# Kernel tuning notes

Hardware: AMD Instinct MI355X
Metric: run time of the kernel (lower is better)

The kernel has to match this reference:

```python
import jax, jax.numpy as jnp
import numpy as np

N, IN_DIM, SLOT_DIM, HID = 524288, 64, 64, 128
NUM_SLOTS, NUM_ITERS = 3, 2
EPS = 1e-8


def _ln(x, g, b):
    m = jnp.mean(x, -1, keepdims=True)
    v = jnp.mean((x - m) ** 2, -1, keepdims=True)
    return (x - m) * jax.lax.rsqrt(v + 1e-5) * g + b


def _gru(x, h, wih, whh, bih, bhh):
    # torch.nn.GRUCell: gates ordered (r, z, n)
    gi = x @ wih.T + bih
    gh = h @ whh.T + bhh
    ir, iz, inn = jnp.split(gi, 3, -1)
    hr, hz, hn = jnp.split(gh, 3, -1)
    r = jax.nn.sigmoid(ir + hr)
    z = jax.nn.sigmoid(iz + hz)
    n = jnp.tanh(inn + r * hn)
    return (1.0 - z) * n + z * h


def setup_inputs() -> dict:
    key = jax.random.key(0)
    ks = jax.random.split(key, 40)
    f32 = jnp.float32
    d = {}
    d['x'] = jax.random.normal(ks[0], (N, IN_DIM), f32)
    d['noise_fg'] = jax.random.normal(ks[1], (NUM_SLOTS - 1, SLOT_DIM), f32)
    d['noise_bg'] = jax.random.normal(ks[2], (1, SLOT_DIM), f32)
    d['ln_in_g'] = jnp.ones((IN_DIM,), f32); d['ln_in_b'] = jnp.zeros((IN_DIM,), f32)
    d['mu_fg'] = jax.random.normal(ks[3], (1, SLOT_DIM), f32)
    d['logsig_fg'] = jax.random.normal(ks[4], (1, SLOT_DIM), f32) * 0.1
    d['mu_bg'] = jax.random.normal(ks[5], (1, SLOT_DIM), f32)
    d['logsig_bg'] = jax.random.normal(ks[6], (1, SLOT_DIM), f32) * 0.1
    d['Wk'] = jax.random.normal(ks[7], (SLOT_DIM, IN_DIM), f32) * 0.1
    d['Wv'] = jax.random.normal(ks[8], (SLOT_DIM, IN_DIM), f32) * 0.1
    d['lnq_fg_g'] = jnp.ones((SLOT_DIM,), f32); d['lnq_fg_b'] = jnp.zeros((SLOT_DIM,), f32)
    d['Wq_fg'] = jax.random.normal(ks[9], (SLOT_DIM, SLOT_DIM), f32) * 0.1
    d['lnq_bg_g'] = jnp.ones((SLOT_DIM,), f32); d['lnq_bg_b'] = jnp.zeros((SLOT_DIM,), f32)
    d['Wq_bg'] = jax.random.normal(ks[10], (SLOT_DIM, SLOT_DIM), f32) * 0.1
    d['gfg_wih'] = jax.random.normal(ks[11], (3 * SLOT_DIM, SLOT_DIM), f32) * 0.1
    d['gfg_whh'] = jax.random.normal(ks[12], (3 * SLOT_DIM, SLOT_DIM), f32) * 0.1
    d['gfg_bih'] = jnp.zeros((3 * SLOT_DIM,), f32); d['gfg_bhh'] = jnp.zeros((3 * SLOT_DIM,), f32)
    d['gbg_wih'] = jax.random.normal(ks[13], (3 * SLOT_DIM, SLOT_DIM), f32) * 0.1
    d['gbg_whh'] = jax.random.normal(ks[14], (3 * SLOT_DIM, SLOT_DIM), f32) * 0.1
    d['gbg_bih'] = jnp.zeros((3 * SLOT_DIM,), f32); d['gbg_bhh'] = jnp.zeros((3 * SLOT_DIM,), f32)
    d['mfg_ln_g'] = jnp.ones((SLOT_DIM,), f32); d['mfg_ln_b'] = jnp.zeros((SLOT_DIM,), f32)
    d['mfg_w1'] = jax.random.normal(ks[15], (HID, SLOT_DIM), f32) * 0.1
    d['mfg_b1'] = jnp.zeros((HID,), f32)
    d['mfg_w2'] = jax.random.normal(ks[16], (SLOT_DIM, HID), f32) * 0.1
    d['mfg_b2'] = jnp.zeros((SLOT_DIM,), f32)
    d['mbg_ln_g'] = jnp.ones((SLOT_DIM,), f32); d['mbg_ln_b'] = jnp.zeros((SLOT_DIM,), f32)
    d['mbg_w1'] = jax.random.normal(ks[17], (HID, SLOT_DIM), f32) * 0.1
    d['mbg_b1'] = jnp.zeros((HID,), f32)
    d['mbg_w2'] = jax.random.normal(ks[18], (SLOT_DIM, HID), f32) * 0.1
    d['mbg_b2'] = jnp.zeros((SLOT_DIM,), f32)
    return d


def _forward(x, noise_fg, noise_bg, ln_in_g, ln_in_b, mu_fg, logsig_fg, mu_bg, logsig_bg,
             Wk, Wv, lnq_fg_g, lnq_fg_b, Wq_fg, lnq_bg_g, lnq_bg_b, Wq_bg,
             gfg_wih, gfg_whh, gfg_bih, gfg_bhh, gbg_wih, gbg_whh, gbg_bih, gbg_bhh,
             mfg_ln_g, mfg_ln_b, mfg_w1, mfg_b1, mfg_w2, mfg_b2,
             mbg_ln_g, mbg_ln_b, mbg_w1, mbg_b1, mbg_w2, mbg_b2):
    scale = SLOT_DIM ** -0.5
    slot_fg = mu_fg + jnp.exp(logsig_fg) * noise_fg        # [K-1, D]
    slot_bg = mu_bg + jnp.exp(logsig_bg) * noise_bg        # [1, D]
    xn = _ln(x, ln_in_g, ln_in_b)
    k = xn @ Wk.T                                          # [N, D]
    v = xn @ Wv.T                                          # [N, D]
    attn = None
    for _ in range(NUM_ITERS):
        q_fg = (_ln(slot_fg, lnq_fg_g, lnq_fg_b) @ Wq_fg.T) * scale
        q_bg = (_ln(slot_bg, lnq_bg_g, lnq_bg_b) @ Wq_bg.T) * scale
        logits = jnp.concatenate([k @ q_bg.T, k @ q_fg.T], axis=-1)  # [N, K]
        attn = jax.nn.softmax(logits, axis=-1)
        attn_bg, attn_fg = attn[:, 0:1], attn[:, 1:]
        w_bg = attn_bg + EPS
        w_bg = w_bg / jnp.sum(w_bg, axis=-2, keepdims=True)
        upd_bg = w_bg.T @ v                                # [1, D]
        w_fg = attn_fg + EPS
        w_fg = w_fg / jnp.sum(w_fg, axis=-2, keepdims=True)
        upd_fg = w_fg.T @ v                                # [K-1, D]
        slot_bg = _gru(upd_bg, slot_bg, gbg_wih, gbg_whh, gbg_bih, gbg_bhh)
        slot_fg = _gru(upd_fg, slot_fg, gfg_wih, gfg_whh, gfg_bih, gfg_bhh)
        slot_bg = slot_bg + (jax.nn.relu(_ln(slot_bg, mbg_ln_g, mbg_ln_b) @ mbg_w1.T + mbg_b1) @ mbg_w2.T + mbg_b2)
        slot_fg = slot_fg + (jax.nn.relu(_ln(slot_fg, mfg_ln_g, mfg_ln_b) @ mfg_w1.T + mfg_b1) @ mfg_w2.T + mfg_b2)
    slots = jnp.concatenate([slot_bg, slot_fg], axis=0)    # [K, D]
    return slots, attn.T                                   # [K,D], [K,N]


def reference(x, noise_fg, noise_bg, ln_in_g, ln_in_b, mu_fg, logsig_fg, mu_bg, logsig_bg,
              Wk, Wv, lnq_fg_g, lnq_fg_b, Wq_fg, lnq_bg_g, lnq_bg_b, Wq_bg,
              gfg_wih, gfg_whh, gfg_bih, gfg_bhh, gbg_wih, gbg_whh, gbg_bih, gbg_bhh,
              mfg_ln_g, mfg_ln_b, mfg_w1, mfg_b1, mfg_w2, mfg_b2,
              mbg_ln_g, mbg_ln_b, mbg_w1, mbg_b1, mbg_w2, mbg_b2):
    return _forward(x, noise_fg, noise_bg, ln_in_g, ln_in_b, mu_fg, logsig_fg, mu_bg, logsig_bg,
                    Wk, Wv, lnq_fg_g, lnq_fg_b, Wq_fg, lnq_bg_g, lnq_bg_b, Wq_bg,
                    gfg_wih, gfg_whh, gfg_bih, gfg_bhh, gbg_wih, gbg_whh, gbg_bih, gbg_bhh,
                    mfg_ln_g, mfg_ln_b, mfg_w1, mfg_b1, mfg_w2, mfg_b2,
                    mbg_ln_g, mbg_ln_b, mbg_w1, mbg_b1, mbg_w2, mbg_b2)
```

## Files before the change

kernel.cpp:

```cpp
#include <hip/hip_runtime.h>
#include <math.h>

#define NROWS 524288
constexpr float EPSW = 1e-8f;

constexpr int OFF_WVT     = 0;
constexpr int OFF_WIHT_BG = 4096;
constexpr int OFF_WHHT_BG = 16384;
constexpr int OFF_WIHT_FG = 28672;
constexpr int OFF_WHHT_FG = 40960;
constexpr int OFF_W1T_BG  = 53248;
constexpr int OFF_W2T_BG  = 61440;
constexpr int OFF_W1T_FG  = 69632;
constexpr int OFF_W2T_FG  = 77824;
constexpr int OFF_WQT_BG  = 86016;
constexpr int OFF_WQT_FG  = 90112;
constexpr int OFF_SLOTS   = 94208;
constexpr int OFF_QG      = 94400;
constexpr int OFF_QS      = 94784;
constexpr int OFF_M       = 94800;
constexpr int OFF_W       = 95184;
constexpr int OFF_CM      = 95190;

__device__ __forceinline__ float wave_sum(float v) {
#pragma unroll
  for (int m = 1; m < 64; m <<= 1) v += __shfl_xor(v, m, 64);
  return v;
}

struct TJob { const float* src; int RC; int Cshift; int dstOff; };
struct TArgs { TJob j[11]; };

__global__ void transpose_k(TArgs a, float* __restrict__ ws) {
  TJob jb = a.j[blockIdx.x];
  const int C = 1 << jb.Cshift;
  const int R = jb.RC >> jb.Cshift;
  float* dst = ws + jb.dstOff;
  for (int e = threadIdx.x; e < jb.RC; e += blockDim.x) {
    int r = e >> jb.Cshift;
    int c = e & (C - 1);
    dst[c * R + r] = jb.src[e];
  }
}

__device__ void emit_q(int lane, float snew,
                       const float* __restrict__ lnq_g, const float* __restrict__ lnq_b,
                       const float* __restrict__ WqT, const float* __restrict__ Wk,
                       const float* __restrict__ g_in, const float* __restrict__ b_in,
                       float* scratch ,
                       float* __restrict__ qg_out , float* __restrict__ qs_out , int s)
{
  float mean = wave_sum(snew) * (1.0f / 64.0f);
  float d = snew - mean;
  float var = wave_sum(d * d) * (1.0f / 64.0f);
  float lns = d * rsqrtf(var + 1e-5f) * lnq_g[lane] + lnq_b[lane];
  scratch[lane] = lns;
  float q = 0.f;
#pragma unroll
  for (int dd = 0; dd < 64; ++dd) q = fmaf(scratch[dd], WqT[dd * 64 + lane], q);
  q *= 0.125f;
  scratch[lane] = q;
  float qk = 0.f;
#pragma unroll
  for (int j = 0; j < 64; ++j) qk = fmaf(scratch[j], Wk[j * 64 + lane], qk);
  float qgv = qk * g_in[lane];
  qg_out[lane] = qgv;
  float QG = wave_sum(qgv);
  float QB = wave_sum(qk * b_in[lane]);
  if (lane == 0) { qs_out[s] = QG; qs_out[3 + s] = QB; }
}

__global__ void init_k(const float* __restrict__ noise_fg, const float* __restrict__ noise_bg,
                       const float* __restrict__ g_in, const float* __restrict__ b_in,
                       const float* __restrict__ mu_fg, const float* __restrict__ logsig_fg,
                       const float* __restrict__ mu_bg, const float* __restrict__ logsig_bg,
                       const float* __restrict__ lnq_fg_g, const float* __restrict__ lnq_fg_b,
                       const float* __restrict__ lnq_bg_g, const float* __restrict__ lnq_bg_b,
                       const float* __restrict__ Wk, float* __restrict__ ws)
{
  __shared__ float scratch[64];
  const int lane = threadIdx.x;
#pragma unroll
  for (int i = 0; i < 6; ++i) ws[OFF_M + i * 64 + lane] = 0.f;
  if (lane < 12) ws[OFF_W + lane] = 0.f;

  float s0 = mu_bg[lane] + __expf(logsig_bg[lane]) * noise_bg[lane];
  float s1 = mu_fg[lane] + __expf(logsig_fg[lane]) * noise_fg[lane];
  float s2 = mu_fg[lane] + __expf(logsig_fg[lane]) * noise_fg[64 + lane];
  ws[OFF_SLOTS + lane] = s0;
  ws[OFF_SLOTS + 64 + lane] = s1;
  ws[OFF_SLOTS + 128 + lane] = s2;

  emit_q(lane, s0, lnq_bg_g, lnq_bg_b, ws + OFF_WQT_BG, Wk, g_in, b_in, scratch,
         ws + OFF_QG + 0, ws + OFF_QS, 0);
  emit_q(lane, s1, lnq_fg_g, lnq_fg_b, ws + OFF_WQT_FG, Wk, g_in, b_in, scratch,
         ws + OFF_QG + 64, ws + OFF_QS, 1);
  emit_q(lane, s2, lnq_fg_g, lnq_fg_b, ws + OFF_WQT_FG, Wk, g_in, b_in, scratch,
         ws + OFF_QG + 128, ws + OFF_QS, 2);
}

template <int WRITE_OUT>
__launch_bounds__(192) __global__ void attn_pass_k(
    const float* __restrict__ x,
    const float* __restrict__ qg,
    const float* __restrict__ qs,
    float* __restrict__ M_out,
    float* __restrict__ W_out,
    float* __restrict__ CM_out,
    float* __restrict__ attn_out)
{
  __shared__ float  lx[3][64 * 65];
  __shared__ float4 lc[3][64];
  __shared__ float4 lqg4[48];
  __shared__ float  lsc[3][8];
  const int tid = threadIdx.x;
  const int wid = tid >> 6, lane = tid & 63;
  if (tid < 48) lqg4[tid] = ((const float4*)qg)[tid];
  __syncthreads();
  const float QG0 = qs[0], QG1 = qs[1], QG2 = qs[2];
  const float QB0 = qs[3], QB1 = qs[4], QB2 = qs[5];

  float accM0 = 0, accM1 = 0, accM2 = 0;
  float accW0 = 0, accW1 = 0, accW2 = 0;
  float accC0 = 0, accC1 = 0, accC2 = 0;
  float* lxw = lx[wid];
  const int nw = gridDim.x * 3;

  for (int chunk = blockIdx.x * 3 + wid; chunk < (NROWS / 64); chunk += nw) {
    const int n0 = chunk << 6;
    const float4* xp = (const float4*)(x + (size_t)n0 * 64);
#pragma unroll
    for (int i = 0; i < 16; ++i) {
      float4 v = xp[i * 64 + lane];
      int f = (i * 64 + lane) << 2;
      float* p = &lxw[(f >> 6) * 65 + (f & 63)];
      p[0] = v.x; p[1] = v.y; p[2] = v.z; p[3] = v.w;
    }
    const float* rowp = &lxw[lane * 65];
    float sum = 0.f, ssq = 0.f, da0 = 0.f, da1 = 0.f, da2 = 0.f;
#pragma unroll
    for (int i = 0; i < 16; ++i) {
      float x0 = rowp[4 * i], x1 = rowp[4 * i + 1], x2 = rowp[4 * i + 2], x3 = rowp[4 * i + 3];
      float4 q0 = lqg4[i], q1 = lqg4[16 + i], q2 = lqg4[32 + i];
      sum += (x0 + x1) + (x2 + x3);
      ssq = fmaf(x0, x0, fmaf(x1, x1, fmaf(x2, x2, fmaf(x3, x3, ssq))));
      da0 = fmaf(x0, q0.x, fmaf(x1, q0.y, fmaf(x2, q0.z, fmaf(x3, q0.w, da0))));
      da1 = fmaf(x0, q1.x, fmaf(x1, q1.y, fmaf(x2, q1.z, fmaf(x3, q1.w, da1))));
      da2 = fmaf(x0, q2.x, fmaf(x1, q2.y, fmaf(x2, q2.z, fmaf(x3, q2.w, da2))));
    }
    float mean = sum * 0.015625f;
    float var  = fmaf(ssq, 0.015625f, -mean * mean);
    float rs   = rsqrtf(var + 1e-5f);
    float l0 = fmaf(rs, da0 - mean * QG0, QB0);
    float l1 = fmaf(rs, da1 - mean * QG1, QB1);
    float l2 = fmaf(rs, da2 - mean * QG2, QB2);
    float mx = fmaxf(l0, fmaxf(l1, l2));
    float e0 = __expf(l0 - mx), e1 = __expf(l1 - mx), e2 = __expf(l2 - mx);
    float inv = 1.0f / (e0 + e1 + e2);
    float a0 = e0 * inv, a1 = e1 * inv, a2 = e2 * inv;
    if (WRITE_OUT) {
      attn_out[0 * NROWS + n0 + lane] = a0;
      attn_out[1 * NROWS + n0 + lane] = a1;
      attn_out[2 * NROWS + n0 + lane] = a2;
    }
    float aw0 = a0 + EPSW, aw1 = a1 + EPSW, aw2 = a2 + EPSW;
    accW0 += aw0; accW1 += aw1; accW2 += aw2;
    float c0 = aw0 * rs, c1 = aw1 * rs, c2 = aw2 * rs;
    accC0 = fmaf(c0, mean, accC0);
    accC1 = fmaf(c1, mean, accC1);
    accC2 = fmaf(c2, mean, accC2);
    lc[wid][lane] = make_float4(c0, c1, c2, 0.f);
#pragma unroll
    for (int r = 0; r < 64; ++r) {
      float4 c = lc[wid][r];
      float xv = lxw[r * 65 + lane];
      accM0 = fmaf(c.x, xv, accM0);
      accM1 = fmaf(c.y, xv, accM1);
      accM2 = fmaf(c.z, xv, accM2);
    }
  }

  accW0 = wave_sum(accW0); accW1 = wave_sum(accW1); accW2 = wave_sum(accW2);
  accC0 = wave_sum(accC0); accC1 = wave_sum(accC1); accC2 = wave_sum(accC2);
  if (lane == 0) {
    lsc[wid][0] = accW0; lsc[wid][1] = accW1; lsc[wid][2] = accW2;
    lsc[wid][3] = accC0; lsc[wid][4] = accC1; lsc[wid][5] = accC2;
  }
  __syncthreads();
  float* red = (float*)lc;
  red[wid * 192 + lane]        = accM0;
  red[wid * 192 + 64 + lane]   = accM1;
  red[wid * 192 + 128 + lane]  = accM2;
  __syncthreads();
  if (tid < 192) atomicAdd(&M_out[tid], red[tid] + red[192 + tid] + red[384 + tid]);
  if (tid < 6) {
    float v = lsc[0][tid] + lsc[1][tid] + lsc[2][tid];
    if (tid < 3) atomicAdd(&W_out[tid], v);
    else         atomicAdd(&CM_out[tid - 3], v);
  }
}

__launch_bounds__(192) __global__ void update_k(
    const float* __restrict__ g_in, const float* __restrict__ b_in,
    const float* __restrict__ gbg_bih, const float* __restrict__ gbg_bhh,
    const float* __restrict__ gfg_bih, const float* __restrict__ gfg_bhh,
    const float* __restrict__ mbg_ln_g, const float* __restrict__ mbg_ln_b,
    const float* __restrict__ mfg_ln_g, const float* __restrict__ mfg_ln_b,
    const float* __restrict__ mbg_b1, const float* __restrict__ mbg_b2,
    const float* __restrict__ mfg_b1, const float* __restrict__ mfg_b2,
    const float* __restrict__ lnq_fg_g, const float* __restrict__ lnq_fg_b,
    const float* __restrict__ lnq_bg_g, const float* __restrict__ lnq_bg_b,
    const float* __restrict__ Wk,
    float* __restrict__ ws, int set_in, int last, float* __restrict__ out_slots)
{
  __shared__ float sA[3][64], sU[3][64], sH[3][64], sHid[3][128];
  const int tid = threadIdx.x, wid = tid >> 6, lane = tid & 63;
  const bool bg = (wid == 0);
  const float* wihT = ws + (bg ? OFF_WIHT_BG : OFF_WIHT_FG);
  const float* whhT = ws + (bg ? OFF_WHHT_BG : OFF_WHHT_FG);
  const float* w1T  = ws + (bg ? OFF_W1T_BG : OFF_W1T_FG);
  const float* w2T  = ws + (bg ? OFF_W2T_BG : OFF_W2T_FG);
  const float* WqT  = ws + (bg ? OFF_WQT_BG : OFF_WQT_FG);
  const float* bih = bg ? gbg_bih : gfg_bih;
  const float* bhh = bg ? gbg_bhh : gfg_bhh;
  const float* mlg = bg ? mbg_ln_g : mfg_ln_g;
  const float* mlb = bg ? mbg_ln_b : mfg_ln_b;
  const float* b1  = bg ? mbg_b1 : mfg_b1;
  const float* b2  = bg ? mbg_b2 : mfg_b2;
  const float* lqg = bg ? lnq_bg_g : lnq_fg_g;
  const float* lqb = bg ? lnq_bg_b : lnq_fg_b;

  const float Wsum = ws[OFF_W + set_in * 3 + wid];
  const float CM   = ws[OFF_CM + set_in * 3 + wid];
  const float Mv   = ws[OFF_M + set_in * 192 + wid * 64 + lane];
  float m = g_in[lane] * (Mv - CM) + b_in[lane] * Wsum;
  sA[wid][lane] = m;
  __syncthreads();

  const float* WvT = ws + OFF_WVT;
  float upd = 0.f;
#pragma unroll
  for (int d = 0; d < 64; ++d) upd = fmaf(sA[wid][d], WvT[d * 64 + lane], upd);
  upd /= Wsum;

  float h = ws[OFF_SLOTS + wid * 64 + lane];
  sU[wid][lane] = upd; sH[wid][lane] = h;
  __syncthreads();

  float gi0 = bih[lane], gi1 = bih[64 + lane], gi2 = bih[128 + lane];
  float gh0 = bhh[lane], gh1 = bhh[64 + lane], gh2 = bhh[128 + lane];
#pragma unroll
  for (int d = 0; d < 64; ++d) {
    float u = sU[wid][d], hh = sH[wid][d];
    const float* wi = &wihT[d * 192];
    const float* wh = &whhT[d * 192];
    gi0 = fmaf(u, wi[lane], gi0);
    gi1 = fmaf(u, wi[64 + lane], gi1);
    gi2 = fmaf(u, wi[128 + lane], gi2);
    gh0 = fmaf(hh, wh[lane], gh0);
    gh1 = fmaf(hh, wh[64 + lane], gh1);
    gh2 = fmaf(hh, wh[128 + lane], gh2);
  }
  float r  = 1.f / (1.f + __expf(-(gi0 + gh0)));
  float z  = 1.f / (1.f + __expf(-(gi1 + gh1)));
  float nn = tanhf(fmaf(r, gh2, gi2));
  float hp = (1.f - z) * nn + z * h;

  float mean = wave_sum(hp) * (1.f / 64.f);
  float dv = hp - mean;
  float var = wave_sum(dv * dv) * (1.f / 64.f);
  float lnh = dv * rsqrtf(var + 1e-5f) * mlg[lane] + mlb[lane];
  __syncthreads();
  sA[wid][lane] = lnh;
  __syncthreads();
  float h1a = b1[lane], h1b = b1[64 + lane];
#pragma unroll
  for (int d = 0; d < 64; ++d) {
    float t = sA[wid][d];
    h1a = fmaf(t, w1T[d * 128 + lane], h1a);
    h1b = fmaf(t, w1T[d * 128 + 64 + lane], h1b);
  }
  h1a = fmaxf(h1a, 0.f); h1b = fmaxf(h1b, 0.f);
  sHid[wid][lane] = h1a; sHid[wid][64 + lane] = h1b;
  __syncthreads();
  float o = b2[lane];
#pragma unroll
  for (int j = 0; j < 128; ++j) o = fmaf(sHid[wid][j], w2T[j * 64 + lane], o);
  float snew = hp + o;
  ws[OFF_SLOTS + wid * 64 + lane] = snew;

  if (last) {
    out_slots[wid * 64 + lane] = snew;
  } else {
    int so = set_in ^ 1;
    emit_q(lane, snew, lqg, lqb, WqT, Wk, g_in, b_in, sA[wid],
           ws + OFF_QG + so * 192 + wid * 64, ws + OFF_QS + so * 6, wid);
  }
}

extern "C" void kernel_launch(void* const* d_in, const int* in_sizes, int n_in,
                              void* d_out, int out_size, void* d_ws, size_t ws_size,
                              hipStream_t stream)
{
  (void)in_sizes; (void)n_in; (void)out_size; (void)ws_size;
  const float* x         = (const float*)d_in[0];
  const float* noise_fg  = (const float*)d_in[1];
  const float* noise_bg  = (const float*)d_in[2];
  const float* ln_in_g   = (const float*)d_in[3];
  const float* ln_in_b   = (const float*)d_in[4];
  const float* mu_fg     = (const float*)d_in[5];
  const float* logsig_fg = (const float*)d_in[6];
  const float* mu_bg     = (const float*)d_in[7];
  const float* logsig_bg = (const float*)d_in[8];
  const float* Wk        = (const float*)d_in[9];
  const float* Wv        = (const float*)d_in[10];
  const float* lnq_fg_g  = (const float*)d_in[11];
  const float* lnq_fg_b  = (const float*)d_in[12];
  const float* Wq_fg     = (const float*)d_in[13];
  const float* lnq_bg_g  = (const float*)d_in[14];
  const float* lnq_bg_b  = (const float*)d_in[15];
  const float* Wq_bg     = (const float*)d_in[16];
  const float* gfg_wih   = (const float*)d_in[17];
  const float* gfg_whh   = (const float*)d_in[18];
  const float* gfg_bih   = (const float*)d_in[19];
  const float* gfg_bhh   = (const float*)d_in[20];
  const float* gbg_wih   = (const float*)d_in[21];
  const float* gbg_whh   = (const float*)d_in[22];
  const float* gbg_bih   = (const float*)d_in[23];
  const float* gbg_bhh   = (const float*)d_in[24];
  const float* mfg_ln_g  = (const float*)d_in[25];
  const float* mfg_ln_b  = (const float*)d_in[26];
  const float* mfg_w1    = (const float*)d_in[27];
  const float* mfg_b1    = (const float*)d_in[28];
  const float* mfg_w2    = (const float*)d_in[29];
  const float* mfg_b2    = (const float*)d_in[30];
  const float* mbg_ln_g  = (const float*)d_in[31];
  const float* mbg_ln_b  = (const float*)d_in[32];
  const float* mbg_w1    = (const float*)d_in[33];
  const float* mbg_b1    = (const float*)d_in[34];
  const float* mbg_w2    = (const float*)d_in[35];
  const float* mbg_b2    = (const float*)d_in[36];

  float* ws  = (float*)d_ws;
  float* out = (float*)d_out;

  TArgs ta;
  ta.j[0]  = {Wv,      64 * 64,  6, OFF_WVT};
  ta.j[1]  = {gbg_wih, 192 * 64, 6, OFF_WIHT_BG};
  ta.j[2]  = {gbg_whh, 192 * 64, 6, OFF_WHHT_BG};
  ta.j[3]  = {gfg_wih, 192 * 64, 6, OFF_WIHT_FG};
  ta.j[4]  = {gfg_whh, 192 * 64, 6, OFF_WHHT_FG};
  ta.j[5]  = {mbg_w1,  128 * 64, 6, OFF_W1T_BG};
  ta.j[6]  = {mbg_w2,  64 * 128, 7, OFF_W2T_BG};
  ta.j[7]  = {mfg_w1,  128 * 64, 6, OFF_W1T_FG};
  ta.j[8]  = {mfg_w2,  64 * 128, 7, OFF_W2T_FG};
  ta.j[9]  = {Wq_bg,   64 * 64,  6, OFF_WQT_BG};
  ta.j[10] = {Wq_fg,   64 * 64,  6, OFF_WQT_FG};
  transpose_k<<<11, 256, 0, stream>>>(ta, ws);

  init_k<<<1, 64, 0, stream>>>(noise_fg, noise_bg, ln_in_g, ln_in_b,
                               mu_fg, logsig_fg, mu_bg, logsig_bg,
                               lnq_fg_g, lnq_fg_b, lnq_bg_g, lnq_bg_b, Wk, ws);

  attn_pass_k<0><<<768, 192, 0, stream>>>(x, ws + OFF_QG, ws + OFF_QS,
                                          ws + OFF_M, ws + OFF_W, ws + OFF_CM, nullptr);
  update_k<<<1, 192, 0, stream>>>(ln_in_g, ln_in_b, gbg_bih, gbg_bhh, gfg_bih, gfg_bhh,
                                  mbg_ln_g, mbg_ln_b, mfg_ln_g, mfg_ln_b,
                                  mbg_b1, mbg_b2, mfg_b1, mfg_b2,
                                  lnq_fg_g, lnq_fg_b, lnq_bg_g, lnq_bg_b, Wk,
                                  ws, 0, 0, nullptr);
  attn_pass_k<1><<<768, 192, 0, stream>>>(x, ws + OFF_QG + 192, ws + OFF_QS + 6,
                                          ws + OFF_M + 192, ws + OFF_W + 3, ws + OFF_CM + 3,
                                          out + 192);
  update_k<<<1, 192, 0, stream>>>(ln_in_g, ln_in_b, gbg_bih, gbg_bhh, gfg_bih, gfg_bhh,
                                  mbg_ln_g, mbg_ln_b, mfg_ln_g, mfg_ln_b,
                                  mbg_b1, mbg_b2, mfg_b1, mfg_b2,
                                  lnq_fg_g, lnq_fg_b, lnq_bg_g, lnq_bg_b, Wk,
                                  ws, 1, 1, out);
}
```

Measured before the change: 527.6 us.

## Restructure attention pass into register-resident streaming and fuse slot update via last-block

The attention pass drops its LDS transpose of x. Each row is now split across 16 lanes holding float4 values, reduced with xor-shuffles, and the next chunk is prefetched into registers, using 1024 blocks of 256 threads. The per-iteration slot update (GRU, MLP, next query) now runs inside the attention kernel: a done-counter atomic picks the last block to do it. The transpose and init kernels are merged into one prep kernel, which also transposes Wq in shared memory. This cuts kernel launches and LDS traffic, at the cost of more shuffles, higher register pressure, and a serialized tail in the final block.

```diff
diff --git a/kernel.cpp b/kernel.cpp
--- a/kernel.cpp
+++ b/kernel.cpp
@@ -21,6 +21,7 @@
 constexpr int OFF_M       = 94800;
 constexpr int OFF_W       = 95184;
 constexpr int OFF_CM      = 95190;
+constexpr int OFF_DONE    = 95200;
 
 __device__ __forceinline__ float wave_sum(float v) {
 #pragma unroll
@@ -28,27 +29,12 @@
   return v;
 }
 
-struct TJob { const float* src; int RC; int Cshift; int dstOff; };
-struct TArgs { TJob j[11]; };
-
-__global__ void transpose_k(TArgs a, float* __restrict__ ws) {
-  TJob jb = a.j[blockIdx.x];
-  const int C = 1 << jb.Cshift;
-  const int R = jb.RC >> jb.Cshift;
-  float* dst = ws + jb.dstOff;
-  for (int e = threadIdx.x; e < jb.RC; e += blockDim.x) {
-    int r = e >> jb.Cshift;
-    int c = e & (C - 1);
-    dst[c * R + r] = jb.src[e];
-  }
-}
-
 __device__ void emit_q(int lane, float snew,
                        const float* __restrict__ lnq_g, const float* __restrict__ lnq_b,
-                       const float* __restrict__ WqT, const float* __restrict__ Wk,
+                       const float* WqT, int qstride, const float* __restrict__ Wk,
                        const float* __restrict__ g_in, const float* __restrict__ b_in,
-                       float* scratch ,
-                       float* __restrict__ qg_out , float* __restrict__ qs_out , int s)
+                       float* scratch,
+                       float* __restrict__ qg_out, float* __restrict__ qs_out, int s)
 {
   float mean = wave_sum(snew) * (1.0f / 64.0f);
   float d = snew - mean;
@@ -56,12 +42,12 @@
   float lns = d * rsqrtf(var + 1e-5f) * lnq_g[lane] + lnq_b[lane];
   scratch[lane] = lns;
   float q = 0.f;
-#pragma unroll
-  for (int dd = 0; dd < 64; ++dd) q = fmaf(scratch[dd], WqT[dd * 64 + lane], q);
+#pragma unroll 8
+  for (int dd = 0; dd < 64; ++dd) q = fmaf(scratch[dd], WqT[dd * qstride + lane], q);
   q *= 0.125f;
   scratch[lane] = q;
   float qk = 0.f;
-#pragma unroll
+#pragma unroll 8
   for (int j = 0; j < 64; ++j) qk = fmaf(scratch[j], Wk[j * 64 + lane], qk);
   float qgv = qk * g_in[lane];
   qg_out[lane] = qgv;
@@ -70,232 +56,296 @@
   if (lane == 0) { qs_out[s] = QG; qs_out[3 + s] = QB; }
 }
 
-__global__ void init_k(const float* __restrict__ noise_fg, const float* __restrict__ noise_bg,
+struct TJob { const float* src; int RC; int Cshift; int dstOff; };
+struct TArgs { TJob j[11]; };
+
+__global__ void prep_k(TArgs a,
+                       const float* __restrict__ noise_fg, const float* __restrict__ noise_bg,
                        const float* __restrict__ g_in, const float* __restrict__ b_in,
                        const float* __restrict__ mu_fg, const float* __restrict__ logsig_fg,
                        const float* __restrict__ mu_bg, const float* __restrict__ logsig_bg,
                        const float* __restrict__ lnq_fg_g, const float* __restrict__ lnq_fg_b,
                        const float* __restrict__ lnq_bg_g, const float* __restrict__ lnq_bg_b,
-                       const float* __restrict__ Wk, float* __restrict__ ws)
+                       const float* __restrict__ Wk,
+                       const float* __restrict__ Wq_bg, const float* __restrict__ Wq_fg,
+                       float* __restrict__ ws)
 {
+  __shared__ float wqT[2][64 * 65];
   __shared__ float scratch[64];
-  const int lane = threadIdx.x;
-#pragma unroll
-  for (int i = 0; i < 6; ++i) ws[OFF_M + i * 64 + lane] = 0.f;
-  if (lane < 12) ws[OFF_W + lane] = 0.f;
-
-  float s0 = mu_bg[lane] + __expf(logsig_bg[lane]) * noise_bg[lane];
-  float s1 = mu_fg[lane] + __expf(logsig_fg[lane]) * noise_fg[lane];
-  float s2 = mu_fg[lane] + __expf(logsig_fg[lane]) * noise_fg[64 + lane];
-  ws[OFF_SLOTS + lane] = s0;
-  ws[OFF_SLOTS + 64 + lane] = s1;
-  ws[OFF_SLOTS + 128 + lane] = s2;
-
-  emit_q(lane, s0, lnq_bg_g, lnq_bg_b, ws + OFF_WQT_BG, Wk, g_in, b_in, scratch,
-         ws + OFF_QG + 0, ws + OFF_QS, 0);
-  emit_q(lane, s1, lnq_fg_g, lnq_fg_b, ws + OFF_WQT_FG, Wk, g_in, b_in, scratch,
-         ws + OFF_QG + 64, ws + OFF_QS, 1);
-  emit_q(lane, s2, lnq_fg_g, lnq_fg_b, ws + OFF_WQT_FG, Wk, g_in, b_in, scratch,
-         ws + OFF_QG + 128, ws + OFF_QS, 2);
+  const int b = blockIdx.x, tid = threadIdx.x;
+  if (b < 11) {
+    TJob jb = a.j[b];
+    const int C = 1 << jb.Cshift;
+    const int R = jb.RC >> jb.Cshift;
+    float* dst = ws + jb.dstOff;
+    for (int e = tid; e < jb.RC; e += blockDim.x) {
+      int r = e >> jb.Cshift;
+      int c = e & (C - 1);
+      dst[c * R + r] = jb.src[e];
+    }
+  } else if (b == 11) {
+    for (int i = tid; i < 384; i += 256) ws[OFF_M + i] = 0.f;
+    if (tid < 12) ws[OFF_W + tid] = 0.f;
+    if (tid < 2) ((int*)(ws + OFF_DONE))[tid] = 0;
+  } else {
+    for (int e = tid; e < 4096; e += 256) {
+      int r = e >> 6, c = e & 63;
+      wqT[0][c * 65 + r] = Wq_bg[e];
+      wqT[1][c * 65 + r] = Wq_fg[e];
+    }
+    __syncthreads();
+    if (tid < 64) {
+      const int lane = tid;
+      float s0 = mu_bg[lane] + __expf(logsig_bg[lane]) * noise_bg[lane];
+      float s1 = mu_fg[lane] + __expf(logsig_fg[lane]) * noise_fg[lane];
+      float s2 = mu_fg[lane] + __expf(logsig_fg[lane]) * noise_fg[64 + lane];
+      ws[OFF_SLOTS + lane] = s0;
+      ws[OFF_SLOTS + 64 + lane] = s1;
+      ws[OFF_SLOTS + 128 + lane] = s2;
+      emit_q(lane, s0, lnq_bg_g, lnq_bg_b, wqT[0], 65, Wk, g_in, b_in, scratch,
+             ws + OFF_QG + 0, ws + OFF_QS, 0);
+      emit_q(lane, s1, lnq_fg_g, lnq_fg_b, wqT[1], 65, Wk, g_in, b_in, scratch,
+             ws + OFF_QG + 64, ws + OFF_QS, 1);
+      emit_q(lane, s2, lnq_fg_g, lnq_fg_b, wqT[1], 65, Wk, g_in, b_in, scratch,
+             ws + OFF_QG + 128, ws + OFF_QS, 2);
+    }
+  }
+}
+
+struct FinPtrs {
+  const float *g_in, *b_in, *gbg_bih, *gbg_bhh, *gfg_bih, *gfg_bhh,
+      *mbg_ln_g, *mbg_ln_b, *mfg_ln_g, *mfg_ln_b, *mbg_b1, *mbg_b2, *mfg_b1, *mfg_b2,
+      *lnq_fg_g, *lnq_fg_b, *lnq_bg_g, *lnq_bg_b, *Wk;
+};
+
+__device__ void finalize(int tid, float* __restrict__ ws, int set,
+                         float* __restrict__ out_slots, const FinPtrs fp)
+{
+  __shared__ float sA[3][64], sU[3][64], sH[3][64], sHid[3][128];
+  const int wid = tid >> 6, lane = tid & 63;
+  const bool act = (wid < 3);
+  const bool bg = (wid == 0);
+  float* M_out = ws + OFF_M + set * 192;
+  float* W_out = ws + OFF_W + set * 3;
+  float* CM_out = ws + OFF_CM + set * 3;
+
+  float Wsum = 1.f, h = 0.f;
+  if (act) {
+    Wsum = atomicAdd(&W_out[wid], 0.f);
+    float CM = atomicAdd(&CM_out[wid], 0.f);
+    float Mv = atomicAdd(&M_out[wid * 64 + lane], 0.f);
+    sA[wid][lane] = fp.g_in[lane] * (Mv - CM) + fp.b_in[lane] * Wsum;
+  }
+  __syncthreads();
+  if (act) {
+    const float* WvT = ws + OFF_WVT;
+    float upd = 0.f;
+#pragma unroll 8
+    for (int d = 0; d < 64; ++d) upd = fmaf(sA[wid][d], WvT[d * 64 + lane], upd);
+    upd /= Wsum;
+    h = ws[OFF_SLOTS + wid * 64 + lane];
+    sU[wid][lane] = upd; sH[wid][lane] = h;
+  }
+  __syncthreads();
+  float hp = 0.f, lnh = 0.f;
+  if (act) {
+    const float* wihT = ws + (bg ? OFF_WIHT_BG : OFF_WIHT_FG);
+    const float* whhT = ws + (bg ? OFF_WHHT_BG : OFF_WHHT_FG);
+    const float* bih = bg ? fp.gbg_bih : fp.gfg_bih;
+    const float* bhh = bg ? fp.gbg_bhh : fp.gfg_bhh;
+    float gi0 = bih[lane], gi1 = bih[64 + lane], gi2 = bih[128 + lane];
+    float gh0 = bhh[lane], gh1 = bhh[64 + lane], gh2 = bhh[128 + lane];
+#pragma unroll 8
+    for (int d = 0; d < 64; ++d) {
+      float u = sU[wid][d], hh = sH[wid][d];
+      const float* wi = &wihT[d * 192];
+      const float* wh = &whhT[d * 192];
+      gi0 = fmaf(u, wi[lane], gi0);
+      gi1 = fmaf(u, wi[64 + lane], gi1);
+      gi2 = fmaf(u, wi[128 + lane], gi2);
+      gh0 = fmaf(hh, wh[lane], gh0);
+      gh1 = fmaf(hh, wh[64 + lane], gh1);
+      gh2 = fmaf(hh, wh[128 + lane], gh2);
+    }
+    float r = 1.f / (1.f + __expf(-(gi0 + gh0)));
+    float z = 1.f / (1.f + __expf(-(gi1 + gh1)));
+    float nn = tanhf(fmaf(r, gh2, gi2));
+    hp = (1.f - z) * nn + z * h;
+    float mean = wave_sum(hp) * (1.f / 64.f);
+    float dv = hp - mean;
+    float var = wave_sum(dv * dv) * (1.f / 64.f);
+    const float* mlg = bg ? fp.mbg_ln_g : fp.mfg_ln_g;
+    const float* mlb = bg ? fp.mbg_ln_b : fp.mfg_ln_b;
+    lnh = dv * rsqrtf(var + 1e-5f) * mlg[lane] + mlb[lane];
+  }
+  __syncthreads();
+  if (act) sA[wid][lane] = lnh;
+  __syncthreads();
+  if (act) {
+    const float* w1T = ws + (bg ? OFF_W1T_BG : OFF_W1T_FG);
+    const float* b1 = bg ? fp.mbg_b1 : fp.mfg_b1;
+    float h1a = b1[lane], h1b = b1[64 + lane];
+#pragma unroll 8
+    for (int d = 0; d < 64; ++d) {
+      float t = sA[wid][d];
+      h1a = fmaf(t, w1T[d * 128 + lane], h1a);
+      h1b = fmaf(t, w1T[d * 128 + 64 + lane], h1b);
+    }
+    sHid[wid][lane] = fmaxf(h1a, 0.f);
+    sHid[wid][64 + lane] = fmaxf(h1b, 0.f);
+  }
+  __syncthreads();
+  if (act) {
+    const float* w2T = ws + (bg ? OFF_W2T_BG : OFF_W2T_FG);
+    const float* b2 = bg ? fp.mbg_b2 : fp.mfg_b2;
+    float o = b2[lane];
+#pragma unroll 8
+    for (int j = 0; j < 128; ++j) o = fmaf(sHid[wid][j], w2T[j * 64 + lane], o);
+    float snew = hp + o;
+    ws[OFF_SLOTS + wid * 64 + lane] = snew;
+    if (out_slots) {
+      out_slots[wid * 64 + lane] = snew;
+    } else {
+      const float* lqg = bg ? fp.lnq_bg_g : fp.lnq_fg_g;
+      const float* lqb = bg ? fp.lnq_bg_b : fp.lnq_fg_b;
+      int so = set ^ 1;
+      emit_q(lane, snew, lqg, lqb, ws + (bg ? OFF_WQT_BG : OFF_WQT_FG), 64,
+             fp.Wk, fp.g_in, fp.b_in, sA[wid],
+             ws + OFF_QG + so * 192 + wid * 64, ws + OFF_QS + so * 6, wid);
+    }
+  }
 }
 
 template <int WRITE_OUT>
-__launch_bounds__(192) __global__ void attn_pass_k(
-    const float* __restrict__ x,
-    const float* __restrict__ qg,
-    const float* __restrict__ qs,
-    float* __restrict__ M_out,
-    float* __restrict__ W_out,
-    float* __restrict__ CM_out,
-    float* __restrict__ attn_out)
+__launch_bounds__(256, 4) __global__ void attn_pass_k(
+    const float* __restrict__ x, float* __restrict__ ws, int set,
+    float* __restrict__ attn_out, float* __restrict__ out_slots, FinPtrs fp)
 {
-  __shared__ float  lx[3][64 * 65];
-  __shared__ float4 lc[3][64];
-  __shared__ float4 lqg4[48];
-  __shared__ float  lsc[3][8];
-  const int tid = threadIdx.x;
-  const int wid = tid >> 6, lane = tid & 63;
-  if (tid < 48) lqg4[tid] = ((const float4*)qg)[tid];
-  __syncthreads();
+  constexpr int NBLK = 1024;
+  const float* qg = ws + OFF_QG + set * 192;
+  const float* qs = ws + OFF_QS + set * 6;
+  float* M_out = ws + OFF_M + set * 192;
+  float* W_out = ws + OFF_W + set * 3;
+  float* CM_out = ws + OFF_CM + set * 3;
+  int* done = (int*)(ws + OFF_DONE) + set;
+
+  const int tid = threadIdx.x, wid = tid >> 6, lane = tid & 63;
+  const int sub = lane & 15, grp = lane >> 4;
+  const float4* qgv = (const float4*)qg;
+  const float4 qg0 = qgv[sub], qg1 = qgv[16 + sub], qg2 = qgv[32 + sub];
   const float QG0 = qs[0], QG1 = qs[1], QG2 = qs[2];
   const float QB0 = qs[3], QB1 = qs[4], QB2 = qs[5];
 
-  float accM0 = 0, accM1 = 0, accM2 = 0;
-  float accW0 = 0, accW1 = 0, accW2 = 0;
-  float accC0 = 0, accC1 = 0, accC2 = 0;
-  float* lxw = lx[wid];
-  const int nw = gridDim.x * 3;
-
-  for (int chunk = blockIdx.x * 3 + wid; chunk < (NROWS / 64); chunk += nw) {
-    const int n0 = chunk << 6;
-    const float4* xp = (const float4*)(x + (size_t)n0 * 64);
-#pragma unroll
-    for (int i = 0; i < 16; ++i) {
-      float4 v = xp[i * 64 + lane];
-      int f = (i * 64 + lane) << 2;
-      float* p = &lxw[(f >> 6) * 65 + (f & 63)];
-      p[0] = v.x; p[1] = v.y; p[2] = v.z; p[3] = v.w;
-    }
-    const float* rowp = &lxw[lane * 65];
-    float sum = 0.f, ssq = 0.f, da0 = 0.f, da1 = 0.f, da2 = 0.f;
-#pragma unroll
-    for (int i = 0; i < 16; ++i) {
-      float x0 = rowp[4 * i], x1 = rowp[4 * i + 1], x2 = rowp[4 * i + 2], x3 = rowp[4 * i + 3];
-      float4 q0 = lqg4[i], q1 = lqg4[16 + i], q2 = lqg4[32 + i];
-      sum += (x0 + x1) + (x2 + x3);
-      ssq = fmaf(x0, x0, fmaf(x1, x1, fmaf(x2, x2, fmaf(x3, x3, ssq))));
-      da0 = fmaf(x0, q0.x, fmaf(x1, q0.y, fmaf(x2, q0.z, fmaf(x3, q0.w, da0))));
-      da1 = fmaf(x0, q1.x, fmaf(x1, q1.y, fmaf(x2, q1.z, fmaf(x3, q1.w, da1))));
-      da2 = fmaf(x0, q2.x, fmaf(x1, q2.y, fmaf(x2, q2.z, fmaf(x3, q2.w, da2))));
-    }
-    float mean = sum * 0.015625f;
-    float var  = fmaf(ssq, 0.015625f, -mean * mean);
-    float rs   = rsqrtf(var + 1e-5f);
-    float l0 = fmaf(rs, da0 - mean * QG0, QB0);
-    float l1 = fmaf(rs, da1 - mean * QG1, QB1);
-    float l2 = fmaf(rs, da2 - mean * QG2, QB2);
-    float mx = fmaxf(l0, fmaxf(l1, l2));
-    float e0 = __expf(l0 - mx), e1 = __expf(l1 - mx), e2 = __expf(l2 - mx);
-    float inv = 1.0f / (e0 + e1 + e2);
-    float a0 = e0 * inv, a1 = e1 * inv, a2 = e2 * inv;
-    if (WRITE_OUT) {
-      attn_out[0 * NROWS + n0 + lane] = a0;
-      attn_out[1 * NROWS + n0 + lane] = a1;
-      attn_out[2 * NROWS + n0 + lane] = a2;
-    }
-    float aw0 = a0 + EPSW, aw1 = a1 + EPSW, aw2 = a2 + EPSW;
-    accW0 += aw0; accW1 += aw1; accW2 += aw2;
-    float c0 = aw0 * rs, c1 = aw1 * rs, c2 = aw2 * rs;
-    accC0 = fmaf(c0, mean, accC0);
-    accC1 = fmaf(c1, mean, accC1);
-    accC2 = fmaf(c2, mean, accC2);
-    lc[wid][lane] = make_float4(c0, c1, c2, 0.f);
-#pragma unroll
-    for (int r = 0; r < 64; ++r) {
-      float4 c = lc[wid][r];
-      float xv = lxw[r * 65 + lane];
-      accM0 = fmaf(c.x, xv, accM0);
-      accM1 = fmaf(c.y, xv, accM1);
-      accM2 = fmaf(c.z, xv, accM2);
-    }
-  }
-
-  accW0 = wave_sum(accW0); accW1 = wave_sum(accW1); accW2 = wave_sum(accW2);
-  accC0 = wave_sum(accC0); accC1 = wave_sum(accC1); accC2 = wave_sum(accC2);
+  float aM[3][4] = {};
+  float aW0 = 0, aW1 = 0, aW2 = 0, aC0 = 0, aC1 = 0, aC2 = 0;
+
+  const float4* xb = (const float4*)x;
+  const int gw = blockIdx.x * 4 + wid;
+  float4 cur[8], nxt[8];
+  {
+    const float4* p = xb + (size_t)gw * 512 + lane;
+#pragma unroll
+    for (int i = 0; i < 8; ++i) cur[i] = p[i * 64];
+  }
+#pragma unroll 1
+  for (int step = 0; step < 4; ++step) {
+    const int ch = gw + step * 4096;
+    if (step < 3) {
+      const float4* p = xb + (size_t)(ch + 4096) * 512 + lane;
+#pragma unroll
+      for (int i = 0; i < 8; ++i) nxt[i] = p[i * 64];
+    }
+#pragma unroll
+    for (int i = 0; i < 8; ++i) {
+      const float4 v = cur[i];
+      float s  = (v.x + v.y) + (v.z + v.w);
+      float q2 = fmaf(v.x, v.x, fmaf(v.y, v.y, fmaf(v.z, v.z, v.w * v.w)));
+      float d0 = fmaf(v.x, qg0.x, fmaf(v.y, qg0.y, fmaf(v.z, qg0.z, v.w * qg0.w)));
+      float d1 = fmaf(v.x, qg1.x, fmaf(v.y, qg1.y, fmaf(v.z, qg1.z, v.w * qg1.w)));
+      float d2 = fmaf(v.x, qg2.x, fmaf(v.y, qg2.y, fmaf(v.z, qg2.z, v.w * qg2.w)));
+#pragma unroll
+      for (int m = 1; m < 16; m <<= 1) {
+        s  += __shfl_xor(s, m, 64);
+        q2 += __shfl_xor(q2, m, 64);
+        d0 += __shfl_xor(d0, m, 64);
+        d1 += __shfl_xor(d1, m, 64);
+        d2 += __shfl_xor(d2, m, 64);
+      }
+      float mean = s * 0.015625f;
+      float var  = fmaf(q2, 0.015625f, -mean * mean);
+      float rs   = rsqrtf(var + 1e-5f);
+      float l0 = fmaf(rs, fmaf(-mean, QG0, d0), QB0);
+      float l1 = fmaf(rs, fmaf(-mean, QG1, d1), QB1);
+      float l2 = fmaf(rs, fmaf(-mean, QG2, d2), QB2);
+      float mx = fmaxf(l0, fmaxf(l1, l2));
+      float e0 = __expf(l0 - mx), e1 = __expf(l1 - mx), e2 = __expf(l2 - mx);
+      float inv = 1.0f / (e0 + e1 + e2);
+      float a0 = e0 * inv, a1 = e1 * inv, a2 = e2 * inv;
+      if (WRITE_OUT) {
+        if (sub == 0) {
+          int r = (ch << 5) + i * 4 + grp;
+          attn_out[r] = a0;
+          attn_out[NROWS + r] = a1;
+          attn_out[2 * NROWS + r] = a2;
+        }
+      }
+      float w0 = a0 + EPSW, w1 = a1 + EPSW, w2 = a2 + EPSW;
+      aW0 += w0; aW1 += w1; aW2 += w2;
+      float c0 = w0 * rs, c1 = w1 * rs, c2 = w2 * rs;
+      aC0 = fmaf(c0, mean, aC0);
+      aC1 = fmaf(c1, mean, aC1);
+      aC2 = fmaf(c2, mean, aC2);
+      aM[0][0] = fmaf(c0, v.x, aM[0][0]); aM[0][1] = fmaf(c0, v.y, aM[0][1]);
+      aM[0][2] = fmaf(c0, v.z, aM[0][2]); aM[0][3] = fmaf(c0, v.w, aM[0][3]);
+      aM[1][0] = fmaf(c1, v.x, aM[1][0]); aM[1][1] = fmaf(c1, v.y, aM[1][1]);
+      aM[1][2] = fmaf(c1, v.z, aM[1][2]); aM[1][3] = fmaf(c1, v.w, aM[1][3]);
+      aM[2][0] = fmaf(c2, v.x, aM[2][0]); aM[2][1] = fmaf(c2, v.y, aM[2][1]);
+      aM[2][2] = fmaf(c2, v.z, aM[2][2]); aM[2][3] = fmaf(c2, v.w, aM[2][3]);
+    }
+    if (step < 3) {
+#pragma unroll
+      for (int i = 0; i < 8; ++i) cur[i] = nxt[i];
+    }
+  }
+
+#pragma unroll
+  for (int s2 = 0; s2 < 3; ++s2)
+#pragma unroll
+    for (int j = 0; j < 4; ++j) {
+      float t = aM[s2][j];
+      t += __shfl_xor(t, 16, 64);
+      t += __shfl_xor(t, 32, 64);
+      aM[s2][j] = t;
+    }
+  __shared__ float redM[4][192];
+  __shared__ float redS[4][6];
+  if (grp == 0) {
+#pragma unroll
+    for (int s2 = 0; s2 < 3; ++s2)
+      *reinterpret_cast<float4*>(&redM[wid][s2 * 64 + 4 * sub]) =
+          make_float4(aM[s2][0], aM[s2][1], aM[s2][2], aM[s2][3]);
+  }
+  aW0 = wave_sum(aW0); aW1 = wave_sum(aW1); aW2 = wave_sum(aW2);
+  aC0 = wave_sum(aC0); aC1 = wave_sum(aC1); aC2 = wave_sum(aC2);
   if (lane == 0) {
-    lsc[wid][0] = accW0; lsc[wid][1] = accW1; lsc[wid][2] = accW2;
-    lsc[wid][3] = accC0; lsc[wid][4] = accC1; lsc[wid][5] = accC2;
-  }
-  __syncthreads();
-  float* red = (float*)lc;
-  red[wid * 192 + lane]        = accM0;
-  red[wid * 192 + 64 + lane]   = accM1;
-  red[wid * 192 + 128 + lane]  = accM2;
-  __syncthreads();
-  if (tid < 192) atomicAdd(&M_out[tid], red[tid] + red[192 + tid] + red[384 + tid]);
+    redS[wid][0] = aW0; redS[wid][1] = aW1; redS[wid][2] = aW2;
+    redS[wid][3] = aC0; redS[wid][4] = aC1; redS[wid][5] = aC2;
+  }
+  __syncthreads();
+  if (tid < 192)
+    atomicAdd(&M_out[tid], redM[0][tid] + redM[1][tid] + redM[2][tid] + redM[3][tid]);
   if (tid < 6) {
-    float v = lsc[0][tid] + lsc[1][tid] + lsc[2][tid];
+    float v = (redS[0][tid] + redS[1][tid] + redS[2][tid] + redS[3][tid]) * 0.0625f;
     if (tid < 3) atomicAdd(&W_out[tid], v);
     else         atomicAdd(&CM_out[tid - 3], v);
   }
-}
-
-__launch_bounds__(192) __global__ void update_k(
-    const float* __restrict__ g_in, const float* __restrict__ b_in,
-    const float* __restrict__ gbg_bih, const float* __restrict__ gbg_bhh,
-    const float* __restrict__ gfg_bih, const float* __restrict__ gfg_bhh,
-    const float* __restrict__ mbg_ln_g, const float* __restrict__ mbg_ln_b,
-    const float* __restrict__ mfg_ln_g, const float* __restrict__ mfg_ln_b,
-    const float* __restrict__ mbg_b1, const float* __restrict__ mbg_b2,
-    const float* __restrict__ mfg_b1, const float* __restrict__ mfg_b2,
-    const float* __restrict__ lnq_fg_g, const float* __restrict__ lnq_fg_b,
-    const float* __restrict__ lnq_bg_g, const float* __restrict__ lnq_bg_b,
-    const float* __restrict__ Wk,
-    float* __restrict__ ws, int set_in, int last, float* __restrict__ out_slots)
-{
-  __shared__ float sA[3][64], sU[3][64], sH[3][64], sHid[3][128];
-  const int tid = threadIdx.x, wid = tid >> 6, lane = tid & 63;
-  const bool bg = (wid == 0);
-  const float* wihT = ws + (bg ? OFF_WIHT_BG : OFF_WIHT_FG);
-  const float* whhT = ws + (bg ? OFF_WHHT_BG : OFF_WHHT_FG);
-  const float* w1T  = ws + (bg ? OFF_W1T_BG : OFF_W1T_FG);
-  const float* w2T  = ws + (bg ? OFF_W2T_BG : OFF_W2T_FG);
-  const float* WqT  = ws + (bg ? OFF_WQT_BG : OFF_WQT_FG);
-  const float* bih = bg ? gbg_bih : gfg_bih;
-  const float* bhh = bg ? gbg_bhh : gfg_bhh;
-  const float* mlg = bg ? mbg_ln_g : mfg_ln_g;
-  const float* mlb = bg ? mbg_ln_b : mfg_ln_b;
-  const float* b1  = bg ? mbg_b1 : mfg_b1;
-  const float* b2  = bg ? mbg_b2 : mfg_b2;
-  const float* lqg = bg ? lnq_bg_g : lnq_fg_g;
-  const float* lqb = bg ? lnq_bg_b : lnq_fg_b;
-
-  const float Wsum = ws[OFF_W + set_in * 3 + wid];
-  const float CM   = ws[OFF_CM + set_in * 3 + wid];
-  const float Mv   = ws[OFF_M + set_in * 192 + wid * 64 + lane];
-  float m = g_in[lane] * (Mv - CM) + b_in[lane] * Wsum;
-  sA[wid][lane] = m;
-  __syncthreads();
-
-  const float* WvT = ws + OFF_WVT;
-  float upd = 0.f;
-#pragma unroll
-  for (int d = 0; d < 64; ++d) upd = fmaf(sA[wid][d], WvT[d * 64 + lane], upd);
-  upd /= Wsum;
-
-  float h = ws[OFF_SLOTS + wid * 64 + lane];
-  sU[wid][lane] = upd; sH[wid][lane] = h;
-  __syncthreads();
-
-  float gi0 = bih[lane], gi1 = bih[64 + lane], gi2 = bih[128 + lane];
-  float gh0 = bhh[lane], gh1 = bhh[64 + lane], gh2 = bhh[128 + lane];
-#pragma unroll
-  for (int d = 0; d < 64; ++d) {
-    float u = sU[wid][d], hh = sH[wid][d];
-    const float* wi = &wihT[d * 192];
-    const float* wh = &whhT[d * 192];
-    gi0 = fmaf(u, wi[lane], gi0);
-    gi1 = fmaf(u, wi[64 + lane], gi1);
-    gi2 = fmaf(u, wi[128 + lane], gi2);
-    gh0 = fmaf(hh, wh[lane], gh0);
-    gh1 = fmaf(hh, wh[64 + lane], gh1);
-    gh2 = fmaf(hh, wh[128 + lane], gh2);
-  }
-  float r  = 1.f / (1.f + __expf(-(gi0 + gh0)));
-  float z  = 1.f / (1.f + __expf(-(gi1 + gh1)));
-  float nn = tanhf(fmaf(r, gh2, gi2));
-  float hp = (1.f - z) * nn + z * h;
-
-  float mean = wave_sum(hp) * (1.f / 64.f);
-  float dv = hp - mean;
-  float var = wave_sum(dv * dv) * (1.f / 64.f);
-  float lnh = dv * rsqrtf(var + 1e-5f) * mlg[lane] + mlb[lane];
-  __syncthreads();
-  sA[wid][lane] = lnh;
-  __syncthreads();
-  float h1a = b1[lane], h1b = b1[64 + lane];
-#pragma unroll
-  for (int d = 0; d < 64; ++d) {
-    float t = sA[wid][d];
-    h1a = fmaf(t, w1T[d * 128 + lane], h1a);
-    h1b = fmaf(t, w1T[d * 128 + 64 + lane], h1b);
-  }
-  h1a = fmaxf(h1a, 0.f); h1b = fmaxf(h1b, 0.f);
-  sHid[wid][lane] = h1a; sHid[wid][64 + lane] = h1b;
-  __syncthreads();
-  float o = b2[lane];
-#pragma unroll
-  for (int j = 0; j < 128; ++j) o = fmaf(sHid[wid][j], w2T[j * 64 + lane], o);
-  float snew = hp + o;
-  ws[OFF_SLOTS + wid * 64 + lane] = snew;
-
-  if (last) {
-    out_slots[wid * 64 + lane] = snew;
-  } else {
-    int so = set_in ^ 1;
-    emit_q(lane, snew, lqg, lqb, WqT, Wk, g_in, b_in, sA[wid],
-           ws + OFF_QG + so * 192 + wid * 64, ws + OFF_QS + so * 6, wid);
-  }
+  __threadfence();
+  __shared__ int lastFlag;
+  __syncthreads();
+  if (tid == 0) lastFlag = (atomicAdd(done, 1) == NBLK - 1) ? 1 : 0;
+  __syncthreads();
+  if (!lastFlag) return;
+  finalize(tid, ws, set, out_slots, fp);
 }
 
 extern "C" void kernel_launch(void* const* d_in, const int* in_sizes, int n_in,
@@ -356,25 +406,16 @@
   ta.j[8]  = {mfg_w2,  64 * 128, 7, OFF_W2T_FG};
   ta.j[9]  = {Wq_bg,   64 * 64,  6, OFF_WQT_BG};
   ta.j[10] = {Wq_fg,   64 * 64,  6, OFF_WQT_FG};
-  transpose_k<<<11, 256, 0, stream>>>(ta, ws);
-
-  init_k<<<1, 64, 0, stream>>>(noise_fg, noise_bg, ln_in_g, ln_in_b,
-                               mu_fg, logsig_fg, mu_bg, logsig_bg,
-                               lnq_fg_g, lnq_fg_b, lnq_bg_g, lnq_bg_b, Wk, ws);
-
-  attn_pass_k<0><<<768, 192, 0, stream>>>(x, ws + OFF_QG, ws + OFF_QS,
-                                          ws + OFF_M, ws + OFF_W, ws + OFF_CM, nullptr);
-  update_k<<<1, 192, 0, stream>>>(ln_in_g, ln_in_b, gbg_bih, gbg_bhh, gfg_bih, gfg_bhh,
-                                  mbg_ln_g, mbg_ln_b, mfg_ln_g, mfg_ln_b,
-                                  mbg_b1, mbg_b2, mfg_b1, mfg_b2,
-                                  lnq_fg_g, lnq_fg_b, lnq_bg_g, lnq_bg_b, Wk,
-                                  ws, 0, 0, nullptr);
-  attn_pass_k<1><<<768, 192, 0, stream>>>(x, ws + OFF_QG + 192, ws + OFF_QS + 6,
-                                          ws + OFF_M + 192, ws + OFF_W + 3, ws + OFF_CM + 3,
-                                          out + 192);
-  update_k<<<1, 192, 0, stream>>>(ln_in_g, ln_in_b, gbg_bih, gbg_bhh, gfg_bih, gfg_bhh,
-                                  mbg_ln_g, mbg_ln_b, mfg_ln_g, mfg_ln_b,
-                                  mbg_b1, mbg_b2, mfg_b1, mfg_b2,
-                                  lnq_fg_g, lnq_fg_b, lnq_bg_g, lnq_bg_b, Wk,
-                                  ws, 1, 1, out);
-}
+
+  prep_k<<<13, 256, 0, stream>>>(ta, noise_fg, noise_bg, ln_in_g, ln_in_b,
+                                 mu_fg, logsig_fg, mu_bg, logsig_bg,
+                                 lnq_fg_g, lnq_fg_b, lnq_bg_g, lnq_bg_b,
+                                 Wk, Wq_bg, Wq_fg, ws);
+
+  FinPtrs fp = {ln_in_g, ln_in_b, gbg_bih, gbg_bhh, gfg_bih, gfg_bhh,
+                mbg_ln_g, mbg_ln_b, mfg_ln_g, mfg_ln_b, mbg_b1, mbg_b2, mfg_b1, mfg_b2,
+                lnq_fg_g, lnq_fg_b, lnq_bg_g, lnq_bg_b, Wk};
+
+  attn_pass_k<0><<<1024, 256, 0, stream>>>(x, ws, 0, nullptr, nullptr, fp);
+  attn_pass_k<1><<<1024, 256, 0, stream>>>(x, ws, 1, out + 192, out, fp);
+}
```

Result: slower. 837.7 us (+58.8%).
